# Performance work log

Measured on AMD Instinct MI355X. Metric: run time of the kernel, lower is better.

## Reference

```python
import jax, jax.numpy as jnp
import numpy as np

B, T, V, D, H, A = 256, 512, 50000, 256, 256, 128


def setup_inputs() -> dict:
    key = jax.random.key(0)
    ks = jax.random.split(key, 9)
    x = jax.random.randint(ks[0], (B, T), 0, V, dtype=jnp.int32)
    embed_w = jax.random.uniform(ks[1], (V, D), dtype=jnp.float32)          # random_uniform init, non-trainable
    lstm_kernel = jax.random.normal(ks[2], (D + H, 4 * H), dtype=jnp.float32) * 0.05  # BasicLSTMCell kernel [i,j,f,o]
    lstm_bias = jnp.zeros((4 * H,), jnp.float32)
    w_omega = jax.random.normal(ks[3], (H, A), dtype=jnp.float32)
    b_omega = jax.random.normal(ks[4], (A,), dtype=jnp.float32)
    u_omega = jax.random.normal(ks[5], (A,), dtype=jnp.float32)
    w = jax.random.normal(ks[6], (H, 2), dtype=jnp.float32)
    b = jnp.zeros((2,), jnp.float32)
    return {"x": x, "embed_w": embed_w, "lstm_kernel": lstm_kernel,
            "lstm_bias": lstm_bias, "w_omega": w_omega, "b_omega": b_omega,
            "u_omega": u_omega, "w": w, "b": b}


def _lstm_attention_forward(x, embed_w, lstm_kernel, lstm_bias, w_omega, b_omega, u_omega, w, b):
    Bt, Tt = x.shape
    Hh = lstm_bias.shape[0] // 4
    seq_len = jnp.sum(jnp.sign(x), axis=1)                         # [B] like tf.reduce_sum(tf.sign(x))
    e = embed_w[x]                                                  # [B,T,D] embedding lookup
    # dynamic_rnn semantics: outputs zeroed past seq_len, state frozen
    mask = (jnp.arange(Tt)[:, None] < seq_len[None, :]).astype(e.dtype)  # [T,B]
    xs = (jnp.transpose(e, (1, 0, 2)), mask[:, :, None])            # time-major

    def step(carry, inp):
        c, h = carry
        x_t, m = inp                                                # [B,D], [B,1]
        z = jnp.concatenate([x_t, h], axis=-1) @ lstm_kernel + lstm_bias  # [B,4H]
        i, j, f, o = jnp.split(z, 4, axis=-1)
        c_new = c * jax.nn.sigmoid(f + 1.0) + jax.nn.sigmoid(i) * jnp.tanh(j)  # forget_bias=1.0
        h_new = jnp.tanh(c_new) * jax.nn.sigmoid(o)
        c = jnp.where(m > 0, c_new, c)
        h_out = h_new * m
        h = jnp.where(m > 0, h_new, h)
        return (c, h), h_out

    c0 = jnp.zeros((Bt, Hh), e.dtype)
    h0 = jnp.zeros((Bt, Hh), e.dtype)
    _, outs = jax.lax.scan(step, (c0, h0), xs)                      # [T,B,H]
    outs = jnp.transpose(outs, (1, 0, 2))                           # [B,T,H]

    # additive attention pooling
    value = jnp.tanh(jnp.einsum('bth,ha->bta', outs, w_omega) + b_omega)
    vu = jnp.einsum('bta,a->bt', value, u_omega)
    alphas = jax.nn.softmax(vu, axis=-1)                            # [B,T]
    last = jnp.sum(outs * alphas[..., None], axis=1)                # [B,H]

    logits = last @ w + b                                           # [B,2]
    return jax.nn.softmax(logits)


def reference(x, embed_w, lstm_kernel, lstm_bias, w_omega, b_omega, u_omega, w, b):
    return _lstm_attention_forward(x, embed_w, lstm_kernel, lstm_bias,
                                   w_omega, b_omega, u_omega, w, b)
```

## Files before the change

kernel.cpp:

```cpp
#include <hip/hip_runtime.h>
#include <hip/hip_bf16.h>
#include <cstdint>
#include <cstddef>

typedef _Float16 f16;
typedef _Float16 f16x8 __attribute__((ext_vector_type(8)));
typedef _Float16 f16x4 __attribute__((ext_vector_type(4)));
typedef float f32x4 __attribute__((ext_vector_type(4)));
typedef unsigned long long u64;
typedef unsigned int u32;

#define B_   256
#define T_   512
#define V_   50000
#define D_   256
#define H_   256
#define A_   128
#define N4H  1024

__device__ __forceinline__ float sigmoid_f(float x) {
    return __builtin_amdgcn_rcpf(1.f + __expf(-x));
}
__device__ __forceinline__ float tanh_f(float x) {
    float e = __expf(-2.f * fabsf(x));
    float t = 1.f - 2.f * e * __builtin_amdgcn_rcpf(1.f + e);
    return copysignf(t, x);
}

#define MFMA_A(accv, afragv, bfraga)                                         \
    asm volatile("v_mfma_f32_16x16x32_f16 %0, %1, %2, %0"                    \
                 : "+v"(accv) : "v"(afragv), "a"(bfraga))

__global__ __launch_bounds__(256) void k0_convert(
    const float* __restrict__ lstm_kernel, const float* __restrict__ w_omega,
    f16* __restrict__ WxT, f16* __restrict__ WhT, f16* __restrict__ WomT) {
    int blk = blockIdx.x;
    int tau = threadIdx.x;
    if (blk < N4H) {
        int n = blk;
        WxT[n * 256 + tau] = (f16)lstm_kernel[(size_t)tau * N4H + n];
        WhT[n * 256 + tau] = (f16)lstm_kernel[(size_t)(256 + tau) * N4H + n];
    } else {
        int a = blk - N4H;
        WomT[a * 256 + tau] = (f16)w_omega[(size_t)tau * A_ + a];
    }
}

__global__ __launch_bounds__(256) void k1_seqlen(
    const int* __restrict__ x, int* __restrict__ seqlen) {
    __shared__ int red[256];
    int b = blockIdx.x, tau = threadIdx.x;
    int cnt = (x[b * T_ + tau] != 0) + (x[b * T_ + tau + 256] != 0);
    red[tau] = cnt;
    __syncthreads();
    for (int s = 128; s > 0; s >>= 1) {
        if (tau < s) red[tau] += red[tau + s];
        __syncthreads();
    }
    if (tau == 0) seqlen[b] = red[0];
}

__global__ __launch_bounds__(256) void k2_zx(
    const int* __restrict__ x, const float* __restrict__ embed,
    const f16* __restrict__ WxT, const float* __restrict__ bias,
    f16* __restrict__ Zx, int t0, int Tc) {
    __shared__ __align__(16) f16 A_s[64][264];
    __shared__ __align__(16) f16 B_s[128][72];
    __shared__ int tok_s[64];

    int tau  = threadIdx.x;
    int bm   = blockIdx.x;
    int i0   = bm * 64;
    int wave = tau >> 6, lane = tau & 63;
    int q = lane >> 4, c = lane & 15;

    if (tau < 64) {
        int i  = i0 + tau;
        int bb = i / Tc, tr = i - bb * Tc;
        tok_s[tau] = x[bb * T_ + t0 + tr];
    }
    __syncthreads();

    {
        int r = tau >> 2, quarter = tau & 3;
        const float4* src =
            (const float4*)(embed + (size_t)tok_s[r] * D_ + quarter * 64);
        f16* dst = &A_s[r][quarter * 64];
#pragma unroll
        for (int j = 0; j < 16; j++) {
            float4 v = src[j];
            dst[j * 4 + 0] = (f16)v.x;
            dst[j * 4 + 1] = (f16)v.y;
            dst[j * 4 + 2] = (f16)v.z;
            dst[j * 4 + 3] = (f16)v.w;
        }
    }

    for (int np = 0; np < 8; np++) {
        f32x4 acc[8];
#pragma unroll
        for (int ni = 0; ni < 8; ni++) acc[ni] = (f32x4){0.f, 0.f, 0.f, 0.f};

        for (int kt = 0; kt < 4; kt++) {
            __syncthreads();
            {
                int n = tau >> 1, half = tau & 1;
                const f16x8* src = (const f16x8*)(WxT +
                    (size_t)(np * 128 + n) * 256 + kt * 64 + half * 32);
                f16x8* dst = (f16x8*)&B_s[n][half * 32];
#pragma unroll
                for (int j = 0; j < 4; j++) dst[j] = src[j];
            }
            __syncthreads();
#pragma unroll
            for (int s = 0; s < 2; s++) {
                f16x8 afrag =
                    *(const f16x8*)&A_s[wave * 16 + c][kt * 64 + s * 32 + q * 8];
#pragma unroll
                for (int ni = 0; ni < 8; ni++) {
                    f16x8 bfrag = *(const f16x8*)&B_s[ni * 16 + c][s * 32 + q * 8];
                    acc[ni] = __builtin_amdgcn_mfma_f32_16x16x32_f16(
                        afrag, bfrag, acc[ni], 0, 0, 0);
                }
            }
        }
#pragma unroll
        for (int ni = 0; ni < 8; ni++) {
            int n    = np * 128 + ni * 16 + c;
            int g    = n >> 8, rem = n & 255;
            int half = rem >> 7, colu = rem & 127;
            int np2  = half * 512 + colu * 4 + g;
            float bv = bias[n];
#pragma unroll
            for (int r = 0; r < 4; r++) {
                int row = i0 + wave * 16 + q * 4 + r;
                Zx[(size_t)row * N4H + np2] = (f16)(acc[ni][r] + bv);
            }
        }
    }
}

__global__ __launch_bounds__(512, 2) void k3_lstm(
    const f16* __restrict__ Zx, const f16* __restrict__ WhT,
    const int* __restrict__ seqlen, f16* __restrict__ outs,
    f16* __restrict__ Hstate, float* __restrict__ Cstate,
    u32* __restrict__ Hex, int t0, int Tc, int first, int last) {
    __shared__ __align__(16) f16 Zx_s[2][16][520];
    __shared__ __align__(16) f16 h_s[2][16][264];

    int tau  = threadIdx.x;
    int w    = tau >> 6, lane = tau & 63;
    int q = lane >> 4, c = lane & 15;
    int wgid = blockIdx.x;
    int pair = wgid >> 1, half = wgid & 1;
    int b0 = pair * 16;
    int u0 = half * 128, pu0 = (half ^ 1) * 128;
    int u  = u0 + w * 16 + c;
    int col = w * 16 + c;

    u32* hexw_my = Hex + (size_t)wgid * 2 * 2048;
    u32* hexw_pr = Hex + (size_t)(wgid ^ 1) * 2 * 2048;

    f32x4 wha[4][8];
#pragma unroll
    for (int g = 0; g < 4; g++)
#pragma unroll
        for (int s = 0; s < 8; s++) {
            int kc = (s < 4) ? (half * 4 + s) : ((half ^ 1) * 4 + (s - 4));
            f16x8 f = *(const f16x8*)(WhT +
                (size_t)(g * 256 + u0 + w * 16 + c) * 256 + kc * 32 + q * 8);
            f32x4 t = __builtin_bit_cast(f32x4, f);
            asm volatile("" : "=a"(wha[g][s]) : "0"(t));
        }

    int kOwn = half * 128 + q * 8;
    int kPar = (half ^ 1) * 128 + q * 8;

    int p0 = t0 & 1;
    if (first) {
        for (int idx = tau; idx < 2 * 16 * 264; idx += 512)
            ((f16*)h_s)[idx] = (f16)0.f;
    } else {
        for (int idx = tau; idx < 16 * 256; idx += 512) {
            int r = idx >> 8, k = idx & 255;
            h_s[p0][r][k] = Hstate[(b0 + r) * H_ + k];
        }
    }

    float cst[4];
    f16   hprev[4];
    int   sl[4];
#pragma unroll
    for (int r = 0; r < 4; r++) {
        int row = q * 4 + r;
        cst[r]   = first ? 0.f : Cstate[(b0 + row) * H_ + u];
        hprev[r] = first ? (f16)0.f : Hstate[(b0 + row) * H_ + u];
        sl[r]    = seqlen[b0 + row];
    }

    int r_st = tau >> 5;
    int cc   = (tau & 31) * 16;
    const f16* zxrow = Zx + ((size_t)(b0 + r_st) * Tc) * N4H + half * 512 + cc;

    {
        const f16x8* src = (const f16x8*)zxrow;
        f16x8* dst = (f16x8*)&Zx_s[p0][r_st][cc];
        dst[0] = src[0];
        dst[1] = src[1];
    }
    int rr = tau >> 5;
    int uu = (tau & 31) * 4;

    __syncthreads();

    f32x4 accO[4];
#pragma unroll
    for (int g = 0; g < 4; g++) accO[g] = (f32x4){0.f, 0.f, 0.f, 0.f};
#pragma unroll
    for (int kk = 0; kk < 4; kk++) {
        f16x8 afrag = *(const f16x8*)&h_s[p0][c][kOwn + kk * 32];
#pragma unroll
        for (int g = 0; g < 4; g++) MFMA_A(accO[g], afrag, wha[g][kk]);
    }

    u64 vp0 = 0, vp1 = 0;

    for (int tt = 0; tt < Tc; tt++) {
        int t   = t0 + tt;
        int cur = t & 1, nxt = cur ^ 1;

        int tn = (tt + 1 < Tc) ? tt + 1 : tt;
        const f16x8* psrc = (const f16x8*)(zxrow + (size_t)tn * N4H);
        f16x8 z0 = psrc[0];
        f16x8 z1 = psrc[1];

        if (tt > 0) {
            u32 tagp = (u32)(t & 0xffff);
            const u64* pp = (const u64*)&hexw_pr[cur * 2048 + rr * 128 + uu];
            while (((u32)(vp0 >> 16) & 0xffffu) != tagp ||
                   ((u32)(vp0 >> 48)) != tagp ||
                   ((u32)(vp1 >> 16) & 0xffffu) != tagp ||
                   ((u32)(vp1 >> 48)) != tagp) {
                vp0 = __hip_atomic_load(pp + 0, __ATOMIC_RELAXED,
                                        __HIP_MEMORY_SCOPE_AGENT);
                vp1 = __hip_atomic_load(pp + 1, __ATOMIC_RELAXED,
                                        __HIP_MEMORY_SCOPE_AGENT);
            }
            u64 hw = (u64)(vp0 & 0xffff) | (((vp0 >> 32) & 0xffff) << 16) |
                     ((vp1 & 0xffff) << 32) | (((vp1 >> 32) & 0xffff) << 48);
            *(u64*)&h_s[cur][rr][pu0 + uu] = hw;
        }
        __syncthreads();

#pragma unroll
        for (int kk = 0; kk < 4; kk++) {
            f16x8 afrag = *(const f16x8*)&h_s[cur][c][kPar + kk * 32];
#pragma unroll
            for (int g = 0; g < 4; g++) MFMA_A(accO[g], afrag, wha[g][4 + kk]);
        }

        u32 tag = (u32)((t + 1) & 0xffff);
        f16 ovals[4];
#pragma unroll
        for (int r = 0; r < 4; r++) {
            int row = q * 4 + r;
            f16x4 zv = *(const f16x4*)&Zx_s[cur][row][col * 4];
            float zi = accO[0][r] + (float)zv[0];
            float zj = accO[1][r] + (float)zv[1];
            float zf = accO[2][r] + (float)zv[2];
            float zo = accO[3][r] + (float)zv[3];
            float ig = sigmoid_f(zi);
            float jg = tanh_f(zj);
            float fg = sigmoid_f(zf + 1.f);
            float og = sigmoid_f(zo);
            float cn = cst[r] * fg + ig * jg;
            float hn = tanh_f(cn) * og;
            bool  m  = (t < sl[r]);
            cst[r]   = m ? cn : cst[r];
            f16 hkeep = m ? (f16)hn : hprev[r];
            hprev[r]  = hkeep;
            h_s[nxt][row][u] = hkeep;
            u32 word = (tag << 16) |
                       (u32)(unsigned short)__builtin_bit_cast(short, hkeep);
            __hip_atomic_store(&hexw_my[nxt * 2048 + row * 128 + col], word,
                               __ATOMIC_RELAXED, __HIP_MEMORY_SCOPE_AGENT);
            ovals[r] = m ? (f16)hn : (f16)0.f;
        }

        {
            const u64* pp2 = (const u64*)&hexw_pr[nxt * 2048 + rr * 128 + uu];
            vp0 = __hip_atomic_load(pp2 + 0, __ATOMIC_RELAXED,
                                    __HIP_MEMORY_SCOPE_AGENT);
            vp1 = __hip_atomic_load(pp2 + 1, __ATOMIC_RELAXED,
                                    __HIP_MEMORY_SCOPE_AGENT);
        }

        {
            f16x8* dst = (f16x8*)&Zx_s[nxt][r_st][cc];
            dst[0] = z0;
            dst[1] = z1;
        }

#pragma unroll
        for (int r = 0; r < 4; r++)
            outs[((size_t)(b0 + q * 4 + r) * T_ + t) * H_ + u] = ovals[r];

        __syncthreads();

#pragma unroll
        for (int g = 0; g < 4; g++) accO[g] = (f32x4){0.f, 0.f, 0.f, 0.f};
#pragma unroll
        for (int kk = 0; kk < 4; kk++) {
            f16x8 afrag = *(const f16x8*)&h_s[nxt][c][kOwn + kk * 32];
#pragma unroll
            for (int g = 0; g < 4; g++) MFMA_A(accO[g], afrag, wha[g][kk]);
        }
    }

    if (!last) {
        int parity = (t0 + Tc) & 1;
        for (int idx = tau; idx < 16 * 128; idx += 512) {
            int r = idx >> 7, k = u0 + (idx & 127);
            Hstate[(b0 + r) * H_ + k] = h_s[parity][r][k];
        }
#pragma unroll
        for (int r = 0; r < 4; r++)
            Cstate[(b0 + q * 4 + r) * H_ + u] = cst[r];
    }
}

__global__ __launch_bounds__(256) void k4_attn(
    const f16* __restrict__ outs, const f16* __restrict__ WomT,
    const float* __restrict__ b_omega, const float* __restrict__ u_omega,
    const float* __restrict__ w, const float* __restrict__ bfin,
    float* __restrict__ out) {
    __shared__ __align__(16) f16 A_s[64][264];
    __shared__ __align__(16) f16 val_s[64][132];
    __shared__ float u_s[128];
    __shared__ float vu_s[512];
    __shared__ float red0[256], red1[256];

    int b = blockIdx.x, tau = threadIdx.x;
    int wave = tau >> 6, lane = tau & 63;
    int q = lane >> 4, c = lane & 15;

    if (tau < 128) u_s[tau] = u_omega[tau];
    float bom[8];
#pragma unroll
    for (int ni = 0; ni < 8; ni++) bom[ni] = b_omega[ni * 16 + c];

    for (int ch = 0; ch < 8; ch++) {
        int t0c = ch * 64;
        __syncthreads();
        {
            int r = tau >> 2, seg = tau & 3;
            const f16x8* src =
                (const f16x8*)(outs + ((size_t)b * T_ + t0c + r) * H_ + seg * 64);
            f16x8* dst = (f16x8*)&A_s[r][seg * 64];
#pragma unroll
            for (int j = 0; j < 8; j++) dst[j] = src[j];
        }
        __syncthreads();

        f32x4 acc[8];
#pragma unroll
        for (int ni = 0; ni < 8; ni++) acc[ni] = (f32x4){0.f, 0.f, 0.f, 0.f};
#pragma unroll
        for (int kc = 0; kc < 8; kc++) {
            f16x8 afrag = *(const f16x8*)&A_s[wave * 16 + c][kc * 32 + q * 8];
#pragma unroll
            for (int ni = 0; ni < 8; ni++) {
                f16x8 bfrag = *(const f16x8*)(WomT +
                    (size_t)(ni * 16 + c) * 256 + kc * 32 + q * 8);
                acc[ni] = __builtin_amdgcn_mfma_f32_16x16x32_f16(
                    afrag, bfrag, acc[ni], 0, 0, 0);
            }
        }
#pragma unroll
        for (int ni = 0; ni < 8; ni++) {
#pragma unroll
            for (int r = 0; r < 4; r++) {
                val_s[wave * 16 + q * 4 + r][ni * 16 + c] =
                    (f16)tanh_f(acc[ni][r] + bom[ni]);
            }
        }
        __syncthreads();
        if (tau < 64) {
            float s = 0.f;
#pragma unroll 8
            for (int a = 0; a < 128; a++) s += (float)val_s[tau][a] * u_s[a];
            vu_s[t0c + tau] = s;
        }
    }
    __syncthreads();

    red0[tau] = fmaxf(vu_s[tau], vu_s[tau + 256]);
    __syncthreads();
    for (int s = 128; s > 0; s >>= 1) {
        if (tau < s) red0[tau] = fmaxf(red0[tau], red0[tau + s]);
        __syncthreads();
    }
    float mx = red0[0];
    __syncthreads();
    float e0 = __expf(vu_s[tau] - mx), e1 = __expf(vu_s[tau + 256] - mx);
    red0[tau] = e0 + e1;
    __syncthreads();
    for (int s = 128; s > 0; s >>= 1) {
        if (tau < s) red0[tau] += red0[tau + s];
        __syncthreads();
    }
    float inv = 1.f / red0[0];
    __syncthreads();
    vu_s[tau]       = e0 * inv;
    vu_s[tau + 256] = e1 * inv;
    __syncthreads();

    float lastv = 0.f;
#pragma unroll 4
    for (int t = 0; t < T_; t++)
        lastv += vu_s[t] * (float)outs[((size_t)b * T_ + t) * H_ + tau];

    red0[tau] = lastv * w[tau * 2 + 0];
    red1[tau] = lastv * w[tau * 2 + 1];
    __syncthreads();
    for (int s = 128; s > 0; s >>= 1) {
        if (tau < s) {
            red0[tau] += red0[tau + s];
            red1[tau] += red1[tau + s];
        }
        __syncthreads();
    }
    if (tau == 0) {
        float l0 = red0[0] + bfin[0], l1 = red1[0] + bfin[1];
        float mm = fmaxf(l0, l1);
        float a0 = __expf(l0 - mm), a1 = __expf(l1 - mm);
        float den = a0 + a1;
        out[b * 2 + 0] = a0 / den;
        out[b * 2 + 1] = a1 / den;
    }
}

extern "C" void kernel_launch(void* const* d_in, const int* in_sizes, int n_in,
                              void* d_out, int out_size, void* d_ws,
                              size_t ws_size, hipStream_t stream) {
    const int*   x           = (const int*)d_in[0];
    const float* embed       = (const float*)d_in[1];
    const float* lstm_kernel = (const float*)d_in[2];
    const float* lstm_bias   = (const float*)d_in[3];
    const float* w_omega     = (const float*)d_in[4];
    const float* b_omega     = (const float*)d_in[5];
    const float* u_omega     = (const float*)d_in[6];
    const float* w           = (const float*)d_in[7];
    const float* bfin        = (const float*)d_in[8];
    float*       out         = (float*)d_out;

    char* ws = (char*)d_ws;
    f16*   WxT    = (f16*)(ws + 0);
    f16*   WhT    = (f16*)(ws + 524288);
    f16*   WomT   = (f16*)(ws + 1048576);
    int*   seqlen = (int*)(ws + 1114112);
    f16*   Hstate = (f16*)(ws + 1115136);
    float* Cstate = (float*)(ws + 1246208);
    u32*   Hex    = (u32*)(ws + 1508352);
    f16*   outs   = (f16*)(ws + 2032640);
    f16*   Zx     = (f16*)(ws + 2032640 + 67108864);

    const size_t fixed = 2032640ull + 67108864ull;
    int nch = 1;
    while (nch < 16 && fixed + 268435456ull / (size_t)nch > ws_size) nch <<= 1;
    int Tc = T_ / nch;

    k0_convert<<<1152, 256, 0, stream>>>(lstm_kernel, w_omega, WxT, WhT, WomT);
    k1_seqlen<<<256, 256, 0, stream>>>(x, seqlen);
    for (int chk = 0; chk < nch; chk++) {
        int t0 = chk * Tc;
        k2_zx<<<(B_ * Tc) / 64, 256, 0, stream>>>(x, embed, WxT, lstm_bias, Zx,
                                                  t0, Tc);
        k3_lstm<<<32, 512, 0, stream>>>(Zx, WhT, seqlen, outs, Hstate, Cstate,
                                        Hex, t0, Tc, chk == 0 ? 1 : 0,
                                        chk == nch - 1 ? 1 : 0);
    }
    k4_attn<<<256, 256, 0, stream>>>(outs, WomT, b_omega, u_omega, w, bfin, out);
}
```

Baseline: 1.596 ms.

## Remap LSTM partner workgroups and add fast-path h exchange with sc0 loads

Changes the pairing of the workgroups that split each batch tile so partners are wgid^8 rather than wgid^1, which likely places them on different XCDs or CUs. It adds a second exchange buffer written with plain stores and polled with a single dwordx4 load using the sc0 cache bit, falling back to agent-scope atomic loads after several tries. The speculative prefetch of the next step's h after the compute phase is removed. The aim is to cut latency on the per-timestep cross-workgroup h handoff, at the cost of double writes and reliance on cache coherence details of the plain-store path.

```diff
diff --git a/kernel.cpp b/kernel.cpp
--- a/kernel.cpp
+++ b/kernel.cpp
@@ -9,6 +9,7 @@
 typedef float f32x4 __attribute__((ext_vector_type(4)));
 typedef unsigned long long u64;
 typedef unsigned int u32;
+typedef unsigned int u32x4 __attribute__((ext_vector_type(4)));
 
 #define B_   256
 #define T_   512
@@ -144,7 +145,8 @@
     const f16* __restrict__ Zx, const f16* __restrict__ WhT,
     const int* __restrict__ seqlen, f16* __restrict__ outs,
     f16* __restrict__ Hstate, float* __restrict__ Cstate,
-    u32* __restrict__ Hex, int t0, int Tc, int first, int last) {
+    u32* __restrict__ Hex, u32* __restrict__ Hexf,
+    int t0, int Tc, int first, int last) {
     __shared__ __align__(16) f16 Zx_s[2][16][520];
     __shared__ __align__(16) f16 h_s[2][16][264];
 
@@ -152,14 +154,17 @@
     int w    = tau >> 6, lane = tau & 63;
     int q = lane >> 4, c = lane & 15;
     int wgid = blockIdx.x;
-    int pair = wgid >> 1, half = wgid & 1;
+    int pair = (wgid & 7) | ((wgid >> 4) << 3);
+    int half = (wgid >> 3) & 1;
     int b0 = pair * 16;
     int u0 = half * 128, pu0 = (half ^ 1) * 128;
     int u  = u0 + w * 16 + c;
     int col = w * 16 + c;
 
-    u32* hexw_my = Hex + (size_t)wgid * 2 * 2048;
-    u32* hexw_pr = Hex + (size_t)(wgid ^ 1) * 2 * 2048;
+    u32*       hexS_my = Hex  + (size_t)wgid * 2 * 2048;
+    const u32* hexS_pr = Hex  + (size_t)(wgid ^ 8) * 2 * 2048;
+    u32*       hexF_my = Hexf + (size_t)wgid * 2 * 2048;
+    const u32* hexF_pr = Hexf + (size_t)(wgid ^ 8) * 2 * 2048;
 
     f32x4 wha[4][8];
 #pragma unroll
@@ -223,33 +228,51 @@
         for (int g = 0; g < 4; g++) MFMA_A(accO[g], afrag, wha[g][kk]);
     }
 
-    u64 vp0 = 0, vp1 = 0;
-
     for (int tt = 0; tt < Tc; tt++) {
         int t   = t0 + tt;
         int cur = t & 1, nxt = cur ^ 1;
+
+        if (tt > 0) {
+            u32 tagp = (u32)(t & 0xffff);
+            const u32* fp = hexF_pr + cur * 2048 + rr * 128 + uu;
+            const u64* sp = (const u64*)(hexS_pr + cur * 2048 + rr * 128 + uu);
+            u64 hw;
+            int tries = 0;
+            for (;;) {
+                u32x4 fv;
+                asm volatile("global_load_dwordx4 %0, %1, off sc0\n\t"
+                             "s_waitcnt vmcnt(0)"
+                             : "=&v"(fv) : "v"(fp) : "memory");
+                if ((fv.x >> 16) == tagp && (fv.y >> 16) == tagp &&
+                    (fv.z >> 16) == tagp && (fv.w >> 16) == tagp) {
+                    hw = (u64)(fv.x & 0xffffu) | ((u64)(fv.y & 0xffffu) << 16) |
+                         ((u64)(fv.z & 0xffffu) << 32) |
+                         ((u64)(fv.w & 0xffffu) << 48);
+                    break;
+                }
+                if (++tries > 4) {
+                    u64 s0 = __hip_atomic_load(sp + 0, __ATOMIC_RELAXED,
+                                               __HIP_MEMORY_SCOPE_AGENT);
+                    u64 s1 = __hip_atomic_load(sp + 1, __ATOMIC_RELAXED,
+                                               __HIP_MEMORY_SCOPE_AGENT);
+                    if (((u32)(s0 >> 16) & 0xffffu) == tagp &&
+                        ((u32)(s0 >> 48)) == tagp &&
+                        ((u32)(s1 >> 16) & 0xffffu) == tagp &&
+                        ((u32)(s1 >> 48)) == tagp) {
+                        hw = (s0 & 0xffff) | (((s0 >> 32) & 0xffff) << 16) |
+                             ((s1 & 0xffff) << 32) | (((s1 >> 32) & 0xffff) << 48);
+                        break;
+                    }
+                }
+            }
+            *(u64*)&h_s[cur][rr][pu0 + uu] = hw;
+        }
 
         int tn = (tt + 1 < Tc) ? tt + 1 : tt;
         const f16x8* psrc = (const f16x8*)(zxrow + (size_t)tn * N4H);
         f16x8 z0 = psrc[0];
         f16x8 z1 = psrc[1];
 
-        if (tt > 0) {
-            u32 tagp = (u32)(t & 0xffff);
-            const u64* pp = (const u64*)&hexw_pr[cur * 2048 + rr * 128 + uu];
-            while (((u32)(vp0 >> 16) & 0xffffu) != tagp ||
-                   ((u32)(vp0 >> 48)) != tagp ||
-                   ((u32)(vp1 >> 16) & 0xffffu) != tagp ||
-                   ((u32)(vp1 >> 48)) != tagp) {
-                vp0 = __hip_atomic_load(pp + 0, __ATOMIC_RELAXED,
-                                        __HIP_MEMORY_SCOPE_AGENT);
-                vp1 = __hip_atomic_load(pp + 1, __ATOMIC_RELAXED,
-                                        __HIP_MEMORY_SCOPE_AGENT);
-            }
-            u64 hw = (u64)(vp0 & 0xffff) | (((vp0 >> 32) & 0xffff) << 16) |
-                     ((vp1 & 0xffff) << 32) | (((vp1 >> 32) & 0xffff) << 48);
-            *(u64*)&h_s[cur][rr][pu0 + uu] = hw;
-        }
         __syncthreads();
 
 #pragma unroll
@@ -282,17 +305,10 @@
             h_s[nxt][row][u] = hkeep;
             u32 word = (tag << 16) |
                        (u32)(unsigned short)__builtin_bit_cast(short, hkeep);
-            __hip_atomic_store(&hexw_my[nxt * 2048 + row * 128 + col], word,
+            hexF_my[nxt * 2048 + row * 128 + col] = word;
+            __hip_atomic_store(&hexS_my[nxt * 2048 + row * 128 + col], word,
                                __ATOMIC_RELAXED, __HIP_MEMORY_SCOPE_AGENT);
             ovals[r] = m ? (f16)hn : (f16)0.f;
-        }
-
-        {
-            const u64* pp2 = (const u64*)&hexw_pr[nxt * 2048 + rr * 128 + uu];
-            vp0 = __hip_atomic_load(pp2 + 0, __ATOMIC_RELAXED,
-                                    __HIP_MEMORY_SCOPE_AGENT);
-            vp1 = __hip_atomic_load(pp2 + 1, __ATOMIC_RELAXED,
-                                    __HIP_MEMORY_SCOPE_AGENT);
         }
 
         {
@@ -462,10 +478,11 @@
     f16*   Hstate = (f16*)(ws + 1115136);
     float* Cstate = (float*)(ws + 1246208);
     u32*   Hex    = (u32*)(ws + 1508352);
-    f16*   outs   = (f16*)(ws + 2032640);
-    f16*   Zx     = (f16*)(ws + 2032640 + 67108864);
-
-    const size_t fixed = 2032640ull + 67108864ull;
+    u32*   Hexf   = (u32*)(ws + 2032640);
+    f16*   outs   = (f16*)(ws + 2556928);
+    f16*   Zx     = (f16*)(ws + 2556928 + 67108864);
+
+    const size_t fixed = 2556928ull + 67108864ull;
     int nch = 1;
     while (nch < 16 && fixed + 268435456ull / (size_t)nch > ws_size) nch <<= 1;
     int Tc = T_ / nch;
@@ -477,7 +494,7 @@
         k2_zx<<<(B_ * Tc) / 64, 256, 0, stream>>>(x, embed, WxT, lstm_bias, Zx,
                                                   t0, Tc);
         k3_lstm<<<32, 512, 0, stream>>>(Zx, WhT, seqlen, outs, Hstate, Cstate,
-                                        Hex, t0, Tc, chk == 0 ? 1 : 0,
+                                        Hex, Hexf, t0, Tc, chk == 0 ? 1 : 0,
                                         chk == nch - 1 ? 1 : 0);
     }
     k4_attn<<<256, 256, 0, stream>>>(outs, WomT, b_omega, u_omega, w, bfin, out);
```

Result: slower. 1.796 ms (+12.5%).
